# Kernel tuning notes

Hardware: AMD Instinct MI355X
Metric: run time of the kernel (lower is better)

Reference implementation:

```python
import jax, jax.numpy as jnp
import numpy as np

R, N, F_IN, F_OUT = 8, 40000, 128, 128
E = 160000  # edges per relation


def setup_inputs() -> dict:
    key = jax.random.key(0)
    ks = jax.random.split(key, 10)
    ent_mat = jax.random.normal(ks[0], (N, F_IN), dtype=jnp.float32)
    rel_mat = jax.random.normal(ks[1], (R, F_IN), dtype=jnp.float32)
    edge_src = jax.random.randint(ks[2], (R, E), 0, N, dtype=jnp.int32)
    edge_dst = jax.random.randint(ks[3], (R, E), 0, N, dtype=jnp.int32)
    edge_val = jax.random.uniform(ks[4], (R, E), dtype=jnp.float32)
    # learned params (xavier-ish scale)
    s_e = (6.0 / (F_IN + F_OUT)) ** 0.5
    weight_ent = jax.random.uniform(ks[5], (F_IN, F_OUT), minval=-s_e, maxval=s_e, dtype=jnp.float32)
    proj_w1 = jax.random.uniform(ks[6], (F_IN, F_OUT), minval=-s_e, maxval=s_e, dtype=jnp.float32)
    proj_b1 = jnp.zeros((F_OUT,), dtype=jnp.float32)
    s_2 = (6.0 / (F_OUT + 1)) ** 0.5
    proj_w2 = jax.random.uniform(ks[7], (F_OUT, 1), minval=-s_2, maxval=s_2, dtype=jnp.float32)
    return {"ent_mat": ent_mat, "rel_mat": rel_mat, "edge_src": edge_src,
            "edge_dst": edge_dst, "edge_val": edge_val, "weight_ent": weight_ent,
            "proj_w1": proj_w1, "proj_b1": proj_b1, "proj_w2": proj_w2}


def reference(ent_mat, rel_mat, edge_src, edge_dst, edge_val, weight_ent, proj_w1, proj_b1, proj_w2):
    # Per-relation SpMM: supports[r] = A_r @ ent_mat, via edge-list segment-sum.
    seg = (jnp.arange(R, dtype=jnp.int32)[:, None] * N + edge_src).reshape(-1)  # [R*E]
    msgs = edge_val.reshape(-1, 1) * ent_mat[edge_dst.reshape(-1)]              # [R*E, F_IN]
    supports = jax.ops.segment_sum(msgs, seg, num_segments=R * N).reshape(R, N, F_IN)
    # Relation gate: sigmoid(Linear(Tanh(Linear(rel_mat))))
    h = jnp.tanh(rel_mat @ proj_w1 + proj_b1)      # [R, F_OUT]
    alpha = jax.nn.sigmoid(h @ proj_w2)            # [R, 1]
    alpha = alpha[:, None, :]                      # [R, 1, 1]
    # Weighted matmul + sum over relations (fused via einsum)
    ent_output = jnp.einsum('rnf,fo->no', supports * alpha, weight_ent)  # [N, F_OUT]
    return (ent_output, rel_mat)
```

## Files before the change

### kernel.cpp

```cpp
#include <hip/hip_runtime.h>

#define R_ 8
#define N_ 40000
#define F_ 128
#define E_ 160000
#define NE (R_ * E_)
#define NBUK 313
#define FBLK 320
#define FCHUNK 4000

typedef unsigned short ushort;
typedef unsigned int uint;
typedef __attribute__((ext_vector_type(8))) short bf16x8;
typedef __attribute__((ext_vector_type(4))) float f32x4;

__device__ __forceinline__ ushort f2bf(float x) {
    uint u = __float_as_uint(x);
    return (ushort)((u + 0x7fffu + ((u >> 16) & 1u)) >> 16);
}

__global__ __launch_bounds__(256) void fused_prep(
        const float* __restrict__ ent, const float* __restrict__ W,
        ushort* __restrict__ proj,
        const int* __restrict__ esrc,
        const float* __restrict__ rel, float* __restrict__ out_tail,
        const float* __restrict__ w1, const float* __restrict__ b1,
        const float* __restrict__ w2, float* __restrict__ alpha,
        int* __restrict__ hist) {
    __shared__ float smem[64 * F_];
    const int t = threadIdx.x;
    const int b = blockIdx.x;
    if (b < 625) {
        ushort* Wt = (ushort*)smem;
#pragma unroll
        for (int p = 0; p < 16; ++p) {
            int k = p * 8 + (t >> 5);
            int c4 = (t & 31) * 4;
            float4 wv = *(const float4*)&W[k * F_ + c4];
#pragma unroll
            for (int i = 0; i < 4; ++i) {
                int col = c4 + i;
                float v = (i == 0) ? wv.x : (i == 1) ? wv.y : (i == 2) ? wv.z : wv.w;
                Wt[col * F_ + ((((k >> 3) ^ (col & 7)) << 3) | (k & 7))] = f2bf(v);
            }
        }
        __syncthreads();
        const int wv_ = t >> 6;
        const int lane = t & 63;
        const int m = lane & 15;
        const int q = (lane >> 4) & 3;
        const int row0 = b * 64 + wv_ * 16;
        bf16x8 afrag[4];
        const float* arow = ent + (size_t)(row0 + m) * F_;
#pragma unroll
        for (int kc = 0; kc < 4; ++kc) {
            float4 a0 = *(const float4*)&arow[kc * 32 + q * 8];
            float4 a1 = *(const float4*)&arow[kc * 32 + q * 8 + 4];
            bf16x8 a;
            a[0] = (short)f2bf(a0.x); a[1] = (short)f2bf(a0.y);
            a[2] = (short)f2bf(a0.z); a[3] = (short)f2bf(a0.w);
            a[4] = (short)f2bf(a1.x); a[5] = (short)f2bf(a1.y);
            a[6] = (short)f2bf(a1.z); a[7] = (short)f2bf(a1.w);
            afrag[kc] = a;
        }
        f32x4 acc[8];
#pragma unroll
        for (int ct = 0; ct < 8; ++ct) acc[ct] = (f32x4){0.f, 0.f, 0.f, 0.f};
#pragma unroll
        for (int ct = 0; ct < 8; ++ct) {
            int n = ct * 16 + m;
#pragma unroll
            for (int kc = 0; kc < 4; ++kc) {
                int chunk = kc * 4 + q;
                bf16x8 bfrag = *(const bf16x8*)&Wt[n * F_ + ((chunk ^ (n & 7)) << 3)];
                acc[ct] = __builtin_amdgcn_mfma_f32_16x16x32_bf16(afrag[kc], bfrag, acc[ct], 0, 0, 0);
            }
        }
#pragma unroll
        for (int ct = 0; ct < 8; ++ct) {
#pragma unroll
            for (int reg = 0; reg < 4; ++reg) {
                int row = row0 + q * 4 + reg;
                proj[(size_t)row * F_ + ct * 16 + m] = f2bf(acc[ct][reg]);
            }
        }
    } else if (b == 625) {
        ((float4*)out_tail)[t] = ((const float4*)rel)[t];
    } else if (b < 630) {
        int r = (b - 626) * 2 + (t >> 7);
        int o = t & 127;
        float s = 0.f;
#pragma unroll 8
        for (int f = 0; f < F_; ++f) s += rel[r * F_ + f] * w1[f * F_ + o];
        float h = tanhf(s + b1[o]);
        smem[t] = h * w2[o];
        __syncthreads();
        for (int off = 64; off > 0; off >>= 1) {
            if ((t & 127) < off) smem[t] += smem[t + off];
            __syncthreads();
        }
        if ((t & 127) == 0) alpha[r] = 1.f / (1.f + expf(-smem[t]));
    } else {
        int hb = b - 630;
        int* h = (int*)smem;
        for (int i = t; i < NBUK; i += 256) h[i] = 0;
        __syncthreads();
        int base = hb * FCHUNK;
        for (int i = t; i < FCHUNK; i += 256)
            atomicAdd(&h[esrc[base + i] >> 7], 1);
        __syncthreads();
        for (int i = t; i < NBUK; i += 256) hist[hb * NBUK + i] = h[i];
    }
}

__global__ __launch_bounds__(FBLK) void fillscan_kernel(const int* __restrict__ hist,
                                                        int* __restrict__ blockbase,
                                                        int* __restrict__ total) {
    __shared__ int sc[FBLK];
    int b = blockIdx.x, t = threadIdx.x;
    int own = hist[t * NBUK + b];
    sc[t] = own;
    __syncthreads();
    for (int off = 1; off < FBLK; off <<= 1) {
        int v = (t >= off) ? sc[t - off] : 0;
        __syncthreads();
        sc[t] += v;
        __syncthreads();
    }
    blockbase[b * FBLK + t] = sc[t] - own;
    if (t == FBLK - 1) total[b] = sc[t];
}

__global__ __launch_bounds__(512) void bucketscan_kernel(const int* __restrict__ total,
                                                         int* __restrict__ bucketbase) {
    __shared__ int sc[512];
    int t = threadIdx.x;
    int v = (t < NBUK) ? total[t] : 0;
    sc[t] = v;
    __syncthreads();
    for (int off = 1; off < 512; off <<= 1) {
        int u = (t >= off) ? sc[t - off] : 0;
        __syncthreads();
        sc[t] += u;
        __syncthreads();
    }
    if (t < NBUK) bucketbase[t] = sc[t] - v;
    if (t == NBUK - 1) bucketbase[NBUK] = sc[t];
}

__global__ __launch_bounds__(256) void fillB_kernel(const int* __restrict__ esrc,
                                                    const int* __restrict__ edst,
                                                    const float* __restrict__ eval_,
                                                    const float* __restrict__ alpha,
                                                    const int* __restrict__ blockbase,
                                                    const int* __restrict__ bucketbase,
                                                    uint2* __restrict__ staged) {
    __shared__ int lcnt[NBUK];
    __shared__ int lbase[NBUK];
    int t = threadIdx.x, blk = blockIdx.x;
    for (int i = t; i < NBUK; i += 256) {
        lcnt[i] = 0;
        lbase[i] = bucketbase[i] + blockbase[i * FBLK + blk];
    }
    __syncthreads();
    int base = blk * FCHUNK;
    for (int i = t; i < FCHUNK; i += 256) {
        int e = base + i;
        int s = esrc[e];
        int d = edst[e];
        float w = alpha[e / E_] * eval_[e];
        int bk = s >> 7;
        int rank = atomicAdd(&lcnt[bk], 1);
        staged[lbase[bk] + rank] = make_uint2((uint)d | ((uint)f2bf(w) << 16), (uint)s);
    }
}

__global__ __launch_bounds__(256) void fillC_kernel(const uint2* __restrict__ staged,
                                                    const int* __restrict__ bucketbase,
                                                    int* __restrict__ rowptr,
                                                    uint* __restrict__ sorted) {
    __shared__ int cnt128[128];
    __shared__ int cur[128];
    int b = blockIdx.x, t = threadIdx.x;
    if (t < 128) cnt128[t] = 0;
    __syncthreads();
    int beg = bucketbase[b], end = bucketbase[b + 1];
    for (int k = beg + t; k < end; k += 256)
        atomicAdd(&cnt128[staged[k].y & 127], 1);
    __syncthreads();
    if (t < 128) cur[t] = cnt128[t];
    __syncthreads();
    for (int off = 1; off < 128; off <<= 1) {
        int v = 0;
        if (t < 128 && t >= off) v = cur[t - off];
        __syncthreads();
        if (t < 128) cur[t] += v;
        __syncthreads();
    }
    int excl = 0;
    if (t < 128) {
        excl = beg + cur[t] - cnt128[t];
        rowptr[(b << 7) + t] = excl;
    }
    __syncthreads();
    if (t < 128) cur[t] = excl;
    __syncthreads();
    for (int k = beg + t; k < end; k += 256) {
        uint2 ed = staged[k];
        int pos = atomicAdd(&cur[ed.y & 127], 1);
        sorted[pos] = ed.x;
    }
}

__global__ __launch_bounds__(256) void spmm_kernel(const int* __restrict__ rowptr,
                                                   const uint* __restrict__ sorted,
                                                   const ushort* __restrict__ proj,
                                                   float* __restrict__ out) {
    int wave = (blockIdx.x * 256 + threadIdx.x) >> 6;
    int lane = threadIdx.x & 63;
    int beg = __builtin_amdgcn_readfirstlane(rowptr[wave]);
    int end = __builtin_amdgcn_readfirstlane(rowptr[wave + 1]);
    float accx = 0.f, accy = 0.f;
    int j = beg;
    for (; j + 4 <= end; j += 4) {
        uint e0 = sorted[j], e1 = sorted[j + 1], e2 = sorted[j + 2], e3 = sorted[j + 3];
        uint u0 = *(const uint*)&proj[((e0 & 0xffffu) << 7) + 2 * lane];
        uint u1 = *(const uint*)&proj[((e1 & 0xffffu) << 7) + 2 * lane];
        uint u2 = *(const uint*)&proj[((e2 & 0xffffu) << 7) + 2 * lane];
        uint u3 = *(const uint*)&proj[((e3 & 0xffffu) << 7) + 2 * lane];
        float w0 = __uint_as_float(e0 & 0xffff0000u);
        float w1 = __uint_as_float(e1 & 0xffff0000u);
        float w2 = __uint_as_float(e2 & 0xffff0000u);
        float w3 = __uint_as_float(e3 & 0xffff0000u);
        accx += w0 * __uint_as_float(u0 << 16);
        accy += w0 * __uint_as_float(u0 & 0xffff0000u);
        accx += w1 * __uint_as_float(u1 << 16);
        accy += w1 * __uint_as_float(u1 & 0xffff0000u);
        accx += w2 * __uint_as_float(u2 << 16);
        accy += w2 * __uint_as_float(u2 & 0xffff0000u);
        accx += w3 * __uint_as_float(u3 << 16);
        accy += w3 * __uint_as_float(u3 & 0xffff0000u);
    }
    for (; j < end; ++j) {
        uint e = sorted[j];
        uint u = *(const uint*)&proj[((e & 0xffffu) << 7) + 2 * lane];
        float w = __uint_as_float(e & 0xffff0000u);
        accx += w * __uint_as_float(u << 16);
        accy += w * __uint_as_float(u & 0xffff0000u);
    }
    *(float2*)&out[((size_t)wave << 7) + 2 * lane] = make_float2(accx, accy);
}

extern "C" void kernel_launch(void* const* d_in, const int* in_sizes, int n_in,
                              void* d_out, int out_size, void* d_ws, size_t ws_size,
                              hipStream_t stream) {
    const float* ent   = (const float*)d_in[0];
    const float* rel   = (const float*)d_in[1];
    const int*   esrc  = (const int*)d_in[2];
    const int*   edst  = (const int*)d_in[3];
    const float* eval_ = (const float*)d_in[4];
    const float* went  = (const float*)d_in[5];
    const float* w1    = (const float*)d_in[6];
    const float* b1    = (const float*)d_in[7];
    const float* w2    = (const float*)d_in[8];

    float* out      = (float*)d_out;
    float* out_tail = out + (size_t)N_ * F_;

    char* ws = (char*)d_ws;
    size_t off = 0;
    ushort* proj      = (ushort*)(ws + off); off += (size_t)N_ * F_ * 2;
    float* alpha      = (float*)(ws + off);  off += 256;
    int*   rowptr     = (int*)(ws + off);    off += (size_t)(N_ + 64) * 4;
    uint*  sorted     = (uint*)(ws + off);   off += (size_t)NE * 4;
    uint2* staged     = (uint2*)(ws + off);  off += (size_t)NE * 8;
    int*   hist       = (int*)(ws + off);    off += (size_t)FBLK * NBUK * 4;
    int*   blockbase  = (int*)(ws + off);    off += (size_t)NBUK * FBLK * 4;
    int*   total      = (int*)(ws + off);    off += (size_t)(NBUK + 7) * 4;
    int*   bucketbase = (int*)(ws + off);    off += (size_t)(NBUK + 7) * 4;

    fused_prep<<<950, 256, 0, stream>>>(ent, went, proj, esrc,
                                        rel, out_tail, w1, b1, w2, alpha, hist);
    fillscan_kernel<<<NBUK, FBLK, 0, stream>>>(hist, blockbase, total);
    bucketscan_kernel<<<1, 512, 0, stream>>>(total, bucketbase);
    fillB_kernel<<<FBLK, 256, 0, stream>>>(esrc, edst, eval_, alpha,
                                           blockbase, bucketbase, staged);
    fillC_kernel<<<NBUK, 256, 0, stream>>>(staged, bucketbase, rowptr, sorted);
    spmm_kernel<<<(N_ * 64) / 256, 256, 0, stream>>>(rowptr, sorted, proj, out);
}
```

Measured before the change: 176.5 us.

## Precompute bf16 weight transpose, shrink staged edges, transpose histogram, unroll SpMM by eight

Adds a one-block kernel that converts and transposes the weight matrix to bf16 once in global memory, so the 625 GEMM blocks stop rebuilding it in shared memory and read B fragments straight from global memory. The staged edge array shrinks from 8 to 5 bytes per edge by splitting it into a payload array and a one-byte source-offset array. The histogram layout is transposed so the scan kernel's reads are coalesced. The SpMM gather loop is unrolled to 8 to keep more loads in flight. The trade-offs are an extra kernel launch and GEMM B reads that now go to global memory or cache instead of LDS.

Measured after the change: 192.5 us. 9.1% more time.

```diff
diff --git a/kernel.cpp b/kernel.cpp
--- a/kernel.cpp
+++ b/kernel.cpp
@@ -11,6 +11,7 @@
 
 typedef unsigned short ushort;
 typedef unsigned int uint;
+typedef unsigned char uchar;
 typedef __attribute__((ext_vector_type(8))) short bf16x8;
 typedef __attribute__((ext_vector_type(4))) float f32x4;
 
@@ -19,32 +20,41 @@
     return (ushort)((u + 0x7fffu + ((u >> 16) & 1u)) >> 16);
 }
 
+__global__ __launch_bounds__(256) void wtconv_kernel(const float* __restrict__ W,
+                                                     ushort* __restrict__ Wt) {
+    __shared__ ushort l[128 * 128];
+    int t = threadIdx.x;
+#pragma unroll
+    for (int p = 0; p < 16; ++p) {
+        int idx = p * 256 + t;
+        int k = idx >> 5;
+        int c4 = (idx & 31) * 4;
+        float4 v = ((const float4*)W)[idx];
+        l[(c4 + 0) * 128 + k] = f2bf(v.x);
+        l[(c4 + 1) * 128 + k] = f2bf(v.y);
+        l[(c4 + 2) * 128 + k] = f2bf(v.z);
+        l[(c4 + 3) * 128 + k] = f2bf(v.w);
+    }
+    __syncthreads();
+#pragma unroll
+    for (int p = 0; p < 8; ++p) {
+        int idx = p * 256 + t;
+        ((float4*)Wt)[idx] = ((const float4*)l)[idx];
+    }
+}
+
 __global__ __launch_bounds__(256) void fused_prep(
-        const float* __restrict__ ent, const float* __restrict__ W,
+        const float* __restrict__ ent, const ushort* __restrict__ Wt,
         ushort* __restrict__ proj,
         const int* __restrict__ esrc,
         const float* __restrict__ rel, float* __restrict__ out_tail,
         const float* __restrict__ w1, const float* __restrict__ b1,
         const float* __restrict__ w2, float* __restrict__ alpha,
         int* __restrict__ hist) {
-    __shared__ float smem[64 * F_];
+    __shared__ float smem[1024];
     const int t = threadIdx.x;
     const int b = blockIdx.x;
     if (b < 625) {
-        ushort* Wt = (ushort*)smem;
-#pragma unroll
-        for (int p = 0; p < 16; ++p) {
-            int k = p * 8 + (t >> 5);
-            int c4 = (t & 31) * 4;
-            float4 wv = *(const float4*)&W[k * F_ + c4];
-#pragma unroll
-            for (int i = 0; i < 4; ++i) {
-                int col = c4 + i;
-                float v = (i == 0) ? wv.x : (i == 1) ? wv.y : (i == 2) ? wv.z : wv.w;
-                Wt[col * F_ + ((((k >> 3) ^ (col & 7)) << 3) | (k & 7))] = f2bf(v);
-            }
-        }
-        __syncthreads();
         const int wv_ = t >> 6;
         const int lane = t & 63;
         const int m = lane & 15;
@@ -71,8 +81,7 @@
             int n = ct * 16 + m;
 #pragma unroll
             for (int kc = 0; kc < 4; ++kc) {
-                int chunk = kc * 4 + q;
-                bf16x8 bfrag = *(const bf16x8*)&Wt[n * F_ + ((chunk ^ (n & 7)) << 3)];
+                bf16x8 bfrag = *(const bf16x8*)&Wt[n * F_ + kc * 32 + q * 8];
                 acc[ct] = __builtin_amdgcn_mfma_f32_16x16x32_bf16(afrag[kc], bfrag, acc[ct], 0, 0, 0);
             }
         }
@@ -109,7 +118,7 @@
         for (int i = t; i < FCHUNK; i += 256)
             atomicAdd(&h[esrc[base + i] >> 7], 1);
         __syncthreads();
-        for (int i = t; i < NBUK; i += 256) hist[hb * NBUK + i] = h[i];
+        for (int i = t; i < NBUK; i += 256) hist[i * FBLK + hb] = h[i];
     }
 }
 
@@ -118,7 +127,7 @@
                                                         int* __restrict__ total) {
     __shared__ int sc[FBLK];
     int b = blockIdx.x, t = threadIdx.x;
-    int own = hist[t * NBUK + b];
+    int own = hist[b * FBLK + t];
     sc[t] = own;
     __syncthreads();
     for (int off = 1; off < FBLK; off <<= 1) {
@@ -154,7 +163,8 @@
                                                     const float* __restrict__ alpha,
                                                     const int* __restrict__ blockbase,
                                                     const int* __restrict__ bucketbase,
-                                                    uint2* __restrict__ staged) {
+                                                    uint* __restrict__ payload,
+                                                    uchar* __restrict__ srcb) {
     __shared__ int lcnt[NBUK];
     __shared__ int lbase[NBUK];
     int t = threadIdx.x, blk = blockIdx.x;
@@ -170,12 +180,14 @@
         int d = edst[e];
         float w = alpha[e / E_] * eval_[e];
         int bk = s >> 7;
-        int rank = atomicAdd(&lcnt[bk], 1);
-        staged[lbase[bk] + rank] = make_uint2((uint)d | ((uint)f2bf(w) << 16), (uint)s);
-    }
-}
-
-__global__ __launch_bounds__(256) void fillC_kernel(const uint2* __restrict__ staged,
+        int idx = lbase[bk] + atomicAdd(&lcnt[bk], 1);
+        payload[idx] = (uint)d | ((uint)f2bf(w) << 16);
+        srcb[idx] = (uchar)(s & 127);
+    }
+}
+
+__global__ __launch_bounds__(256) void fillC_kernel(const uint* __restrict__ payload,
+                                                    const uchar* __restrict__ srcb,
                                                     const int* __restrict__ bucketbase,
                                                     int* __restrict__ rowptr,
                                                     uint* __restrict__ sorted) {
@@ -186,7 +198,7 @@
     __syncthreads();
     int beg = bucketbase[b], end = bucketbase[b + 1];
     for (int k = beg + t; k < end; k += 256)
-        atomicAdd(&cnt128[staged[k].y & 127], 1);
+        atomicAdd(&cnt128[srcb[k]], 1);
     __syncthreads();
     if (t < 128) cur[t] = cnt128[t];
     __syncthreads();
@@ -206,9 +218,9 @@
     if (t < 128) cur[t] = excl;
     __syncthreads();
     for (int k = beg + t; k < end; k += 256) {
-        uint2 ed = staged[k];
-        int pos = atomicAdd(&cur[ed.y & 127], 1);
-        sorted[pos] = ed.x;
+        uint pl = payload[k];
+        int pos = atomicAdd(&cur[srcb[k]], 1);
+        sorted[pos] = pl;
     }
 }
 
@@ -222,24 +234,19 @@
     int end = __builtin_amdgcn_readfirstlane(rowptr[wave + 1]);
     float accx = 0.f, accy = 0.f;
     int j = beg;
-    for (; j + 4 <= end; j += 4) {
-        uint e0 = sorted[j], e1 = sorted[j + 1], e2 = sorted[j + 2], e3 = sorted[j + 3];
-        uint u0 = *(const uint*)&proj[((e0 & 0xffffu) << 7) + 2 * lane];
-        uint u1 = *(const uint*)&proj[((e1 & 0xffffu) << 7) + 2 * lane];
-        uint u2 = *(const uint*)&proj[((e2 & 0xffffu) << 7) + 2 * lane];
-        uint u3 = *(const uint*)&proj[((e3 & 0xffffu) << 7) + 2 * lane];
-        float w0 = __uint_as_float(e0 & 0xffff0000u);
-        float w1 = __uint_as_float(e1 & 0xffff0000u);
-        float w2 = __uint_as_float(e2 & 0xffff0000u);
-        float w3 = __uint_as_float(e3 & 0xffff0000u);
-        accx += w0 * __uint_as_float(u0 << 16);
-        accy += w0 * __uint_as_float(u0 & 0xffff0000u);
-        accx += w1 * __uint_as_float(u1 << 16);
-        accy += w1 * __uint_as_float(u1 & 0xffff0000u);
-        accx += w2 * __uint_as_float(u2 << 16);
-        accy += w2 * __uint_as_float(u2 & 0xffff0000u);
-        accx += w3 * __uint_as_float(u3 << 16);
-        accy += w3 * __uint_as_float(u3 & 0xffff0000u);
+    for (; j + 8 <= end; j += 8) {
+        uint e[8], u[8];
+#pragma unroll
+        for (int i = 0; i < 8; ++i) e[i] = sorted[j + i];
+#pragma unroll
+        for (int i = 0; i < 8; ++i)
+            u[i] = *(const uint*)&proj[((e[i] & 0xffffu) << 7) + 2 * lane];
+#pragma unroll
+        for (int i = 0; i < 8; ++i) {
+            float w = __uint_as_float(e[i] & 0xffff0000u);
+            accx += w * __uint_as_float(u[i] << 16);
+            accy += w * __uint_as_float(u[i] & 0xffff0000u);
+        }
     }
     for (; j < end; ++j) {
         uint e = sorted[j];
@@ -270,21 +277,24 @@
     char* ws = (char*)d_ws;
     size_t off = 0;
     ushort* proj      = (ushort*)(ws + off); off += (size_t)N_ * F_ * 2;
-    float* alpha      = (float*)(ws + off);  off += 256;
-    int*   rowptr     = (int*)(ws + off);    off += (size_t)(N_ + 64) * 4;
-    uint*  sorted     = (uint*)(ws + off);   off += (size_t)NE * 4;
-    uint2* staged     = (uint2*)(ws + off);  off += (size_t)NE * 8;
-    int*   hist       = (int*)(ws + off);    off += (size_t)FBLK * NBUK * 4;
-    int*   blockbase  = (int*)(ws + off);    off += (size_t)NBUK * FBLK * 4;
-    int*   total      = (int*)(ws + off);    off += (size_t)(NBUK + 7) * 4;
-    int*   bucketbase = (int*)(ws + off);    off += (size_t)(NBUK + 7) * 4;
-
-    fused_prep<<<950, 256, 0, stream>>>(ent, went, proj, esrc,
+    ushort* Wt        = (ushort*)(ws + off); off += (size_t)F_ * F_ * 2;
+    float*  alpha     = (float*)(ws + off);  off += 256;
+    uint*   payload   = (uint*)(ws + off);   off += (size_t)NE * 4;
+    uchar*  srcb      = (uchar*)(ws + off);  off += (size_t)NE + 256;
+    uint*   sorted    = (uint*)(ws + off);   off += (size_t)NE * 4;
+    int*    rowptr    = (int*)(ws + off);    off += (size_t)(N_ + 64) * 4;
+    int*    hist      = (int*)(ws + off);    off += (size_t)NBUK * FBLK * 4;
+    int*    blockbase = (int*)(ws + off);    off += (size_t)NBUK * FBLK * 4;
+    int*    total     = (int*)(ws + off);    off += (size_t)(NBUK + 7) * 4;
+    int*    bucketbase= (int*)(ws + off);    off += (size_t)(NBUK + 7) * 4;
+
+    wtconv_kernel<<<1, 256, 0, stream>>>(went, Wt);
+    fused_prep<<<950, 256, 0, stream>>>(ent, Wt, proj, esrc,
                                         rel, out_tail, w1, b1, w2, alpha, hist);
     fillscan_kernel<<<NBUK, FBLK, 0, stream>>>(hist, blockbase, total);
     bucketscan_kernel<<<1, 512, 0, stream>>>(total, bucketbase);
     fillB_kernel<<<FBLK, 256, 0, stream>>>(esrc, edst, eval_, alpha,
-                                           blockbase, bucketbase, staged);
-    fillC_kernel<<<NBUK, 256, 0, stream>>>(staged, bucketbase, rowptr, sorted);
+                                           blockbase, bucketbase, payload, srcb);
+    fillC_kernel<<<NBUK, 256, 0, stream>>>(payload, srcb, bucketbase, rowptr, sorted);
     spmm_kernel<<<(N_ * 64) / 256, 256, 0, stream>>>(rowptr, sorted, proj, out);
 }
```
